# Kernel optimization log

Measured on AMD Instinct MI355X. Metric: run time of the kernel, lower is better.

The kernel has to match this reference:

```python
import jax, jax.numpy as jnp
import numpy as np
import math

RATIO = 0.8

def setup_inputs() -> dict:
    key = jax.random.key(0)
    ks = jax.random.split(key, 10)
    N, E, D = 10000, 320000, 256
    h = jax.random.normal(ks[0], (N, D), dtype=jnp.float32)
    edge_index = jax.random.randint(ks[1], (2, E), 0, N, dtype=jnp.int64)
    s = 1.0 / math.sqrt(D)
    # SAGEConv: lin_l (on aggregated neighbors, with bias), lin_r (on self, no bias)
    W_l = jax.random.normal(ks[2], (D, D), dtype=jnp.float32) * s
    b_l = jax.random.normal(ks[3], (D,), dtype=jnp.float32) * s
    W_r = jax.random.normal(ks[4], (D, D), dtype=jnp.float32) * s
    # SAGPooling score GNN = GraphConv(D, 1): lin_rel (aggr, bias), lin_root (self, no bias)
    W_rel = jax.random.normal(ks[5], (D, 1), dtype=jnp.float32) * s
    b_rel = jax.random.normal(ks[6], (1,), dtype=jnp.float32) * s
    W_root = jax.random.normal(ks[7], (D, 1), dtype=jnp.float32) * s
    # GlobalAttention gate_nn = Linear(D, 1)
    W_gate = jax.random.normal(ks[8], (D, 1), dtype=jnp.float32) * s
    b_gate = jax.random.normal(ks[9], (1,), dtype=jnp.float32) * s
    return {"h": h, "edge_index": edge_index, "W_l": W_l, "b_l": b_l,
            "W_r": W_r, "W_rel": W_rel, "b_rel": b_rel, "W_root": W_root,
            "W_gate": W_gate, "b_gate": b_gate}

def reference(h, edge_index, W_l, b_l, W_r, W_rel, b_rel, W_root, W_gate, b_gate):
    N = h.shape[0]
    src, dst = edge_index[0], edge_index[1]
    # ---- SAGEConv (mean aggregation) ----
    agg = jax.ops.segment_sum(h[src], dst, num_segments=N)          # [N, D]
    deg = jax.ops.segment_sum(jnp.ones_like(dst, dtype=h.dtype), dst, num_segments=N)
    mean = agg / jnp.clip(deg, 1.0)[:, None]
    x = jax.nn.relu(mean @ W_l + b_l + h @ W_r)                     # [N, D]
    # ---- SAGPooling: score via GraphConv (add aggregation), tanh, top-k ----
    s_agg = jax.ops.segment_sum(x[src], dst, num_segments=N)        # [N, D]
    score = (s_agg @ W_rel + b_rel + x @ W_root).reshape(-1)        # [N]
    score = jnp.tanh(score)
    k = int(math.ceil(RATIO * N))                                   # static 8000
    top_score, perm = jax.lax.top_k(score, k)
    xp = x[perm] * top_score[:, None]                               # [k, D]
    # ---- GlobalAttention readout (single graph) ----
    gate = jax.nn.softmax(xp @ W_gate + b_gate, axis=0)             # [k, 1]
    out = jnp.sum(gate * xp, axis=0, keepdims=True)                 # [1, D]
    return out
```

## Files before the change

kernel.cpp:

```cpp
#include <hip/hip_runtime.h>
#include <hip/hip_fp8.h>
#include <math.h>

#define NN 10000
#define NE 320000
#define DD 256
#define KSEL 8000
#define KK 512
#define NPART 157

typedef unsigned int uint;
typedef unsigned short ushort;
typedef unsigned char uchar;
typedef __attribute__((ext_vector_type(8))) short short8;
typedef __attribute__((ext_vector_type(4))) float f32x4;
typedef __attribute__((ext_vector_type(4))) ushort us4;
typedef __attribute__((ext_vector_type(8))) ushort us8;

__device__ __forceinline__ uint encodeF(float f) {
    uint u = __float_as_uint(f);
    return (u & 0x80000000u) ? ~u : (u | 0x80000000u);
}

__device__ __forceinline__ ushort f2bf(float f) {
    uint u = __float_as_uint(f);
    u += 0x7FFFu + ((u >> 16) & 1u);
    return (ushort)(u >> 16);
}

__device__ __forceinline__ float fp8dec(uint b) {
    __hip_fp8_e4m3 t;
    t.__x = (__hip_fp8_storage_t)b;
    return (float)t;
}
__device__ __forceinline__ uint fp8enc(float f) {
    return (uint)__hip_fp8_e4m3(f).__x;
}

#define ZQUADS 2504
__global__ __launch_bounds__(256) void zero_bufs(float4* __restrict__ z) {
    int i = blockIdx.x * 256 + threadIdx.x;
    if (i < ZQUADS) z[i] = make_float4(0.f, 0.f, 0.f, 0.f);
}

#define WB 32
#define HB 2500
#define DB 1250
__global__ __launch_bounds__(256) void prep(
    const float* __restrict__ h, const float* __restrict__ W_l,
    const float* __restrict__ W_r, const int* __restrict__ ei,
    ushort* __restrict__ Ab, uchar* __restrict__ h8,
    ushort* __restrict__ Wt, int* __restrict__ degi) {
    const int b = blockIdx.x, t = threadIdx.x;
    if (b < WB) {
        __shared__ float tile[64][65];
        const int tr = b >> 2, tc = b & 3;
        const int k0 = tr * 64, n0 = tc * 64;
        const int r = t >> 6, c = t & 63;
        const float* Wsrc = (k0 < 256) ? (W_l + (size_t)k0 * DD)
                                       : (W_r + (size_t)(k0 - 256) * DD);
#pragma unroll
        for (int i = 0; i < 16; i++) {
            int row = r + i * 4;
            tile[row][c] = Wsrc[(size_t)row * DD + n0 + c];
        }
        __syncthreads();
#pragma unroll
        for (int i = 0; i < 16; i++) {
            int row = r + i * 4;
            Wt[(size_t)(n0 + row) * KK + k0 + c] = f2bf(tile[c][row]);
        }
    } else if (b < WB + HB) {
        int id = (b - WB) * 256 + t;
        int node = id >> 6, seg = (id & 63) * 4;
        float4 v = *(const float4*)(h + (size_t)node * DD + seg);
        us4 o;
        o[0] = f2bf(v.x); o[1] = f2bf(v.y); o[2] = f2bf(v.z); o[3] = f2bf(v.w);
        *(us4*)(Ab + (size_t)node * KK + 256 + seg) = o;
        uint pk = fp8enc(v.x) | (fp8enc(v.y) << 8)
                | (fp8enc(v.z) << 16) | (fp8enc(v.w) << 24);
        *(uint*)(h8 + (size_t)node * DD + seg) = pk;
    } else {
        int e = (b - WB - HB) * 256 + t;
        if (e < NE) atomicAdd(&degi[ei[NE + e]], 1);
    }
}

__global__ __launch_bounds__(1024) void scan_start(
    const int* __restrict__ degi, int* __restrict__ start,
    int* __restrict__ cursor, float* __restrict__ invdeg) {
    __shared__ int wsum[16];
    __shared__ int woff[16];
    const int t = threadIdx.x, wid = t >> 6, lane = t & 63;
    const int CH = 10;
    const int base = t * CH;
    int sum = 0;
#pragma unroll
    for (int i = 0; i < CH; i++) {
        int idx = base + i;
        if (idx < NN) sum += degi[idx];
    }
    int x = sum;
#pragma unroll
    for (int off = 1; off < 64; off <<= 1) {
        int v = __shfl_up(x, off);
        if (lane >= off) x += v;
    }
    if (lane == 63) wsum[wid] = x;
    __syncthreads();
    if (t == 0) {
        int run = 0;
#pragma unroll
        for (int w = 0; w < 16; w++) { woff[w] = run; run += wsum[w]; }
    }
    __syncthreads();
    int run = woff[wid] + x - sum;
#pragma unroll
    for (int i = 0; i < CH; i++) {
        int idx = base + i;
        if (idx < NN) {
            start[idx]  = run;
            cursor[idx] = run;
            int d = degi[idx];
            invdeg[idx] = 1.0f / fmaxf((float)d, 1.0f);
            run += d;
        }
    }
    if (t == 1023) start[NN] = NE;
}

__global__ __launch_bounds__(256) void fill_csr(
    const int* __restrict__ ei, int* __restrict__ cursor,
    int* __restrict__ csr) {
    int e = blockIdx.x * 256 + threadIdx.x;
    if (e >= NE) return;
    int pos = atomicAdd(&cursor[ei[NE + e]], 1);
    csr[pos] = ei[e];
}

__global__ __launch_bounds__(256) void gather_mean(
    ushort* __restrict__ Ab, const uchar* __restrict__ h8,
    const int* __restrict__ csr,
    const int* __restrict__ start, const float* __restrict__ invdeg) {
    int node = blockIdx.x * 4 + (threadIdx.x >> 6);
    int lane = threadIdx.x & 63;
    if (node >= NN) return;
    int s = start[node], e = start[node + 1];
    const uchar* hp = h8 + lane * 4;
    float a0 = 0.f, a1 = 0.f, a2 = 0.f, a3 = 0.f;
    float b0 = 0.f, b1 = 0.f, b2 = 0.f, b3 = 0.f;
    int j = s;
    for (; j + 4 <= e; j += 4) {
        int s0 = csr[j], s1 = csr[j + 1], s2 = csr[j + 2], s3 = csr[j + 3];
        uint w0 = *(const uint*)(hp + (size_t)s0 * DD);
        uint w1 = *(const uint*)(hp + (size_t)s1 * DD);
        uint w2 = *(const uint*)(hp + (size_t)s2 * DD);
        uint w3 = *(const uint*)(hp + (size_t)s3 * DD);
        a0 += fp8dec(w0 & 0xFF) + fp8dec(w1 & 0xFF);
        a1 += fp8dec((w0 >> 8) & 0xFF) + fp8dec((w1 >> 8) & 0xFF);
        a2 += fp8dec((w0 >> 16) & 0xFF) + fp8dec((w1 >> 16) & 0xFF);
        a3 += fp8dec(w0 >> 24) + fp8dec(w1 >> 24);
        b0 += fp8dec(w2 & 0xFF) + fp8dec(w3 & 0xFF);
        b1 += fp8dec((w2 >> 8) & 0xFF) + fp8dec((w3 >> 8) & 0xFF);
        b2 += fp8dec((w2 >> 16) & 0xFF) + fp8dec((w3 >> 16) & 0xFF);
        b3 += fp8dec(w2 >> 24) + fp8dec(w3 >> 24);
    }
    for (; j < e; j++) {
        uint w0 = *(const uint*)(hp + (size_t)csr[j] * DD);
        a0 += fp8dec(w0 & 0xFF);
        a1 += fp8dec((w0 >> 8) & 0xFF);
        a2 += fp8dec((w0 >> 16) & 0xFF);
        a3 += fp8dec(w0 >> 24);
    }
    float id = invdeg[node];
    us4 m;
    m[0] = f2bf((a0 + b0) * id);
    m[1] = f2bf((a1 + b1) * id);
    m[2] = f2bf((a2 + b2) * id);
    m[3] = f2bf((a3 + b3) * id);
    *(us4*)(Ab + (size_t)node * KK + lane * 4) = m;
}

__global__ __launch_bounds__(256) void gemm_x(
    const ushort* __restrict__ Ab, const ushort* __restrict__ Wt,
    const float* __restrict__ b_l,
    const float* __restrict__ W_rel, const float* __restrict__ W_gate,
    const float* __restrict__ W_root,
    float* __restrict__ xout, float* __restrict__ y,
    float* __restrict__ cvec, float* __restrict__ rvec) {
    __shared__ ushort Asm[2][32][40];
    __shared__ ushort Bsm[2][256][40];
    __shared__ float Ys[4][32], Cs[4][32], Rs[4][32];
    const int t    = threadIdx.x;
    const int row0 = blockIdx.x * 32;
    const int wid  = t >> 6, lane = t & 63;
    const int l15  = lane & 15, g = lane >> 4;

    f32x4 acc[2][4];
#pragma unroll
    for (int fi = 0; fi < 2; fi++)
#pragma unroll
        for (int fj = 0; fj < 4; fj++) acc[fi][fj] = (f32x4)0.f;

    const int  arow = t >> 3, akseg = (t & 7) * 4;
    const bool aok  = (row0 + arow) < NN;
    const ushort* aptr = Ab + (size_t)(row0 + arow) * KK + akseg;
    const ushort* bptr = Wt + (size_t)t * KK;

    us4 areg = {0, 0, 0, 0};
    us8 breg[4];
    if (aok) areg = *(const us4*)(aptr);
#pragma unroll
    for (int jj = 0; jj < 4; jj++) breg[jj] = *(const us8*)(bptr + jj * 8);
    *(us4*)&Asm[0][arow][akseg] = areg;
#pragma unroll
    for (int jj = 0; jj < 4; jj++) *(us8*)&Bsm[0][t][jj * 8] = breg[jj];
    __syncthreads();

    for (int ks = 0; ks < 16; ++ks) {
        const int cur = ks & 1;
        if (ks < 15) {
            const int k0 = (ks + 1) * 32;
            if (aok) areg = *(const us4*)(aptr + k0);
#pragma unroll
            for (int jj = 0; jj < 4; jj++) breg[jj] = *(const us8*)(bptr + k0 + jj * 8);
        }
        short8 af0 = *(const short8*)&Asm[cur][l15][g * 8];
        short8 af1 = *(const short8*)&Asm[cur][16 + l15][g * 8];
#pragma unroll
        for (int fj = 0; fj < 4; fj++) {
            short8 bf = *(const short8*)&Bsm[cur][wid * 64 + fj * 16 + l15][g * 8];
            acc[0][fj] = __builtin_amdgcn_mfma_f32_16x16x32_bf16(af0, bf, acc[0][fj], 0, 0, 0);
            acc[1][fj] = __builtin_amdgcn_mfma_f32_16x16x32_bf16(af1, bf, acc[1][fj], 0, 0, 0);
        }
        if (ks < 15) {
            const int nb = cur ^ 1;
            *(us4*)&Asm[nb][arow][akseg] = areg;
#pragma unroll
            for (int jj = 0; jj < 4; jj++) *(us8*)&Bsm[nb][t][jj * 8] = breg[jj];
        }
        __syncthreads();
    }

    const int wcol0 = wid * 64;
    float bl[4], wl[4], wg[4], wo[4];
#pragma unroll
    for (int fj = 0; fj < 4; fj++) {
        int col = wcol0 + fj * 16 + l15;
        bl[fj] = b_l[col]; wl[fj] = W_rel[col];
        wg[fj] = W_gate[col]; wo[fj] = W_root[col];
    }
#pragma unroll
    for (int fi = 0; fi < 2; fi++) {
#pragma unroll
        for (int r = 0; r < 4; r++) {
            int row = row0 + fi * 16 + g * 4 + r;
            float py = 0.f, pc = 0.f, pr = 0.f;
#pragma unroll
            for (int fj = 0; fj < 4; fj++) {
                float v = fmaxf(acc[fi][fj][r] + bl[fj], 0.f);
                if (row < NN)
                    xout[(size_t)row * DD + wcol0 + fj * 16 + l15] = v;
                py = fmaf(v, wl[fj], py);
                pc = fmaf(v, wg[fj], pc);
                pr = fmaf(v, wo[fj], pr);
            }
#pragma unroll
            for (int off = 1; off < 16; off <<= 1) {
                py += __shfl_xor(py, off);
                pc += __shfl_xor(pc, off);
                pr += __shfl_xor(pr, off);
            }
            if (l15 == 0) {
                int rl = fi * 16 + g * 4 + r;
                Ys[wid][rl] = py; Cs[wid][rl] = pc; Rs[wid][rl] = pr;
            }
        }
    }
    __syncthreads();
    if (t < 32) {
        int row = row0 + t;
        if (row < NN) {
            y[row]    = Ys[0][t] + Ys[1][t] + Ys[2][t] + Ys[3][t];
            cvec[row] = Cs[0][t] + Cs[1][t] + Cs[2][t] + Cs[3][t];
            rvec[row] = Rs[0][t] + Rs[1][t] + Rs[2][t] + Rs[3][t];
        }
    }
}

__global__ __launch_bounds__(256) void gather_score(
    const float* __restrict__ y, const float* __restrict__ r,
    const float* __restrict__ b_rel, const int* __restrict__ csr,
    const int* __restrict__ start,
    float* __restrict__ score, uint* __restrict__ key) {
    int gt   = blockIdx.x * 256 + threadIdx.x;
    int node = gt >> 4, l = gt & 15;
    if (node >= NN) return;
    int s = start[node], e = start[node + 1];
    float acc = 0.f;
    for (int j = s + l; j < e; j += 16) acc += y[csr[j]];
#pragma unroll
    for (int o = 8; o; o >>= 1) acc += __shfl_xor(acc, o, 16);
    if (l == 0) {
        float sc = tanhf(acc + b_rel[0] + r[node]);
        score[node] = sc;
        key[node]   = encodeF(sc);
    }
}

__global__ __launch_bounds__(1024) void radix_select(
    const uint* __restrict__ key, const float* __restrict__ score,
    const float* __restrict__ cvec,
    float* __restrict__ wsc, float* __restrict__ denom) {
    __shared__ uint  hist[16][260];
    __shared__ uint  sh_prefix, sh_need;
    __shared__ float wred[16];
    __shared__ uint  tick_s;
    const int t = threadIdx.x, wid = t >> 6, lane = t & 63;

    uint  myk[10];
    float mys[10], myl[10];
#pragma unroll
    for (int i = 0; i < 10; i++) {
        int idx = t + i * 1024;
        if (idx < NN) {
            uint k  = key[idx];
            float s = score[idx];
            myk[i] = k; mys[i] = s; myl[i] = s * cvec[idx];
        } else {
            myk[i] = 0u; mys[i] = 0.f; myl[i] = -INFINITY;
        }
    }

    uint prefix = 0, pmask = 0, need = KSEL;
    float vmax = -INFINITY;
    for (int shift = 24; shift >= 0; shift -= 8) {
        for (int i = lane; i < 256; i += 64) hist[wid][i] = 0;
        if (shift == 0) {
#pragma unroll
            for (int i = 0; i < 10; i++) {
                uint k = myk[i];
                if ((k & pmask) == prefix) atomicAdd(&hist[wid][k & 255], 1u);
                if (k >= prefix) vmax = fmaxf(vmax, myl[i]);
            }
        } else {
#pragma unroll
            for (int i = 0; i < 10; i++) {
                uint k = myk[i];
                if ((k & pmask) == prefix)
                    atomicAdd(&hist[wid][(k >> shift) & 255], 1u);
            }
        }
        __syncthreads();
        if (wid == 0) {
            uint4 a = make_uint4(0u, 0u, 0u, 0u);
#pragma unroll
            for (int w = 0; w < 16; w++) {
                uint4 v = *(const uint4*)&hist[w][lane * 4];
                a.x += v.x; a.y += v.y; a.z += v.z; a.w += v.w;
            }
            uint s3 = a.w, s2 = a.z + s3, s1 = a.y + s2, s0 = a.x + s1;
            uint x = s0;
#pragma unroll
            for (int off = 1; off < 64; off <<= 1) {
                uint v = __shfl_down(x, off);
                if (lane + off < 64) x += v;
            }
            uint excl = x - s0;
            uint hi0 = excl + s0, hi1 = excl + s1;
            uint hi2 = excl + s2, hi3 = excl + s3;
            if (need <= hi0 && need > hi0 - a.x) {
                sh_prefix = prefix | ((uint)(lane * 4 + 0) << shift);
                sh_need   = need - (hi0 - a.x);
            }
            if (need <= hi1 && need > hi1 - a.y) {
                sh_prefix = prefix | ((uint)(lane * 4 + 1) << shift);
                sh_need   = need - (hi1 - a.y);
            }
            if (need <= hi2 && need > hi2 - a.z) {
                sh_prefix = prefix | ((uint)(lane * 4 + 2) << shift);
                sh_need   = need - (hi2 - a.z);
            }
            if (need <= hi3 && need > hi3 - a.w) {
                sh_prefix = prefix | ((uint)(lane * 4 + 3) << shift);
                sh_need   = need - (hi3 - a.w);
            }
        }
        __syncthreads();
        prefix = sh_prefix;
        need   = sh_need;
        pmask |= (0xFFu << shift);
    }
    const uint T      = prefix;
    const uint needEq = need;
#pragma unroll
    for (int o = 32; o; o >>= 1) vmax = fmaxf(vmax, __shfl_xor(vmax, o));
    if (lane == 0) wred[wid] = vmax;
    if (t == 0) tick_s = 0;
    __syncthreads();
    float m = wred[0];
#pragma unroll
    for (int w = 1; w < 16; w++) m = fmaxf(m, wred[w]);
    __syncthreads();
    float dsum = 0.f;
#pragma unroll
    for (int i = 0; i < 10; i++) {
        int idx = t + i * 1024;
        if (idx >= NN) continue;
        uint k = myk[i];
        bool selm = (k > T);
        if (k == T) selm = (atomicAdd(&tick_s, 1u) < needEq);
        float wv = 0.f;
        if (selm) {
            float w = expf(myl[i] - m);
            wv   = w * mys[i];
            dsum += w;
        }
        wsc[idx] = wv;
    }
#pragma unroll
    for (int o = 32; o; o >>= 1) dsum += __shfl_xor(dsum, o);
    if (lane == 0) wred[wid] = dsum;
    __syncthreads();
    if (t == 0) {
        float d = 0.f;
#pragma unroll
        for (int w = 0; w < 16; w++) d += wred[w];
        denom[0] = d;
    }
}

__global__ __launch_bounds__(256) void reduce_rows(
    const float* __restrict__ x, const float* __restrict__ wsc,
    float* __restrict__ part, uint* __restrict__ counter,
    const float* __restrict__ denom, float* __restrict__ out) {
    __shared__ float red[3][DD];
    __shared__ uint  lastdone;
    const int wave = threadIdx.x >> 6;
    const int lane = threadIdx.x & 63;
    const int row0 = (blockIdx.x * 4 + wave) * 16;
    const float* xp = x + lane * 4;
    float4 acc = make_float4(0.f, 0.f, 0.f, 0.f);
    if (row0 < NN) {
#pragma unroll
        for (int rb = 0; rb < 16; rb += 4) {
            int r0 = row0 + rb;
            float w0 = wsc[r0 + 0], w1 = wsc[r0 + 1];
            float w2 = wsc[r0 + 2], w3 = wsc[r0 + 3];
            float4 v0 = *(const float4*)(xp + (size_t)(r0 + 0) * DD);
            float4 v1 = *(const float4*)(xp + (size_t)(r0 + 1) * DD);
            float4 v2 = *(const float4*)(xp + (size_t)(r0 + 2) * DD);
            float4 v3 = *(const float4*)(xp + (size_t)(r0 + 3) * DD);
            acc.x = fmaf(w0, v0.x, fmaf(w1, v1.x, fmaf(w2, v2.x, fmaf(w3, v3.x, acc.x))));
            acc.y = fmaf(w0, v0.y, fmaf(w1, v1.y, fmaf(w2, v2.y, fmaf(w3, v3.y, acc.y))));
            acc.z = fmaf(w0, v0.z, fmaf(w1, v1.z, fmaf(w2, v2.z, fmaf(w3, v3.z, acc.z))));
            acc.w = fmaf(w0, v0.w, fmaf(w1, v1.w, fmaf(w2, v2.w, fmaf(w3, v3.w, acc.w))));
        }
    }
    if (wave > 0) *(float4*)&red[wave - 1][lane * 4] = acc;
    __syncthreads();
    if (wave == 0) {
#pragma unroll
        for (int w = 0; w < 3; w++) {
            float4 rv = *(float4*)&red[w][lane * 4];
            acc.x += rv.x; acc.y += rv.y; acc.z += rv.z; acc.w += rv.w;
        }
        *(float4*)(part + (size_t)blockIdx.x * DD + lane * 4) = acc;
    }
    __threadfence();
    if (threadIdx.x == 0) lastdone = atomicAdd(counter, 1u);
    __syncthreads();
    if (lastdone == NPART - 1) {
        __threadfence();
        int i = threadIdx.x;
        float s = 0.f;
        for (int b = 0; b < NPART; b++) s += part[(size_t)b * DD + i];
        out[i] = s / denom[0];
    }
}

extern "C" void kernel_launch(void* const* d_in, const int* in_sizes, int n_in,
                              void* d_out, int out_size, void* d_ws, size_t ws_size,
                              hipStream_t stream) {
    const float* h      = (const float*)d_in[0];
    const int*   ei     = (const int*)d_in[1];
    const float* W_l    = (const float*)d_in[2];
    const float* b_l    = (const float*)d_in[3];
    const float* W_r    = (const float*)d_in[4];
    const float* W_rel  = (const float*)d_in[5];
    const float* b_rel  = (const float*)d_in[6];
    const float* W_root = (const float*)d_in[7];
    const float* W_gate = (const float*)d_in[8];
    float* out = (float*)d_out;

    char* p = (char*)d_ws;
    auto alloc = [&p](size_t bytes) {
        char* q = p;
        p += (bytes + 63) & ~(size_t)63;
        return q;
    };
    ushort* Ab    = (ushort*)alloc((size_t)NN * KK * 2);
    uchar*  h8    = (uchar*) alloc((size_t)NN * DD);
    float*  xbuf  = (float*) alloc((size_t)NN * DD * 4);
    ushort* Wt    = (ushort*)alloc((size_t)DD * KK * 2);
    int*    csr   = (int*)   alloc((size_t)NE * 4);
    int*    start = (int*)   alloc((size_t)(NN + 1) * 4);
    int*    cursor= (int*)   alloc((size_t)NN * 4);
    float*  invdeg= (float*) alloc((size_t)NN * 4);
    float*  score = (float*) alloc((size_t)NN * 4);
    uint*   key   = (uint*)  alloc((size_t)NN * 4);
    float*  wsc   = (float*) alloc((size_t)NN * 4);
    float*  denom = (float*) alloc(64);
    float*  part  = (float*) alloc((size_t)NPART * DD * 4);
    float*  y     = (float*) alloc((size_t)NN * 4);
    float*  cbuf  = (float*) alloc((size_t)NN * 4);
    float*  rbuf  = (float*) alloc((size_t)NN * 4);
    int*    degi  = (int*)   alloc((size_t)NN * 4);
    uint*   cnt   = (uint*)  alloc(64);

    zero_bufs   <<<(ZQUADS + 255) / 256, 256, 0, stream>>>((float4*)degi);
    prep        <<<WB + HB + DB, 256, 0, stream>>>(h, W_l, W_r, ei,
                                                   Ab, h8, Wt, degi);
    scan_start  <<<1, 1024, 0, stream>>>(degi, start, cursor, invdeg);
    fill_csr    <<<(NE + 255) / 256, 256, 0, stream>>>(ei, cursor, csr);
    gather_mean <<<(NN + 3) / 4, 256, 0, stream>>>(Ab, h8, csr, start, invdeg);
    gemm_x      <<<(NN + 31) / 32, 256, 0, stream>>>(Ab, Wt, b_l,
                                                     W_rel, W_gate, W_root,
                                                     xbuf, y, cbuf, rbuf);
    gather_score<<<(NN * 16 + 255) / 256, 256, 0, stream>>>(y, rbuf, b_rel, csr,
                                                            start, score, key);
    radix_select<<<1, 1024, 0, stream>>>(key, score, cbuf, wsc, denom);
    reduce_rows <<<NPART, 256, 0, stream>>>(xbuf, wsc, part, cnt, denom, out);
    (void)n_in; (void)in_sizes; (void)out_size; (void)ws_size;
}
```

Before: 161.3 us.

## Fuse neighbor mean gather into the GEMM prologue via shared memory

Removes the separate gather_mean kernel. Each gemm_x block now gathers and averages the fp8 neighbor features for its 32 rows into a shared-memory tile, and the first half of the K loop reads that tile. The self-feature half of the A matrix is still staged from global memory, which is now stored with stride DD instead of KK. This avoids one launch and the global write and re-read of the bf16 mean matrix. In exchange, the latency-bound gather runs with far fewer waves (313 blocks, 8 rows per wave done serially), and the extra shared-memory tile may lower occupancy.

New measurement: 191.3 us. 18.6% more time.

```diff
diff --git a/kernel.cpp b/kernel.cpp
--- a/kernel.cpp
+++ b/kernel.cpp
@@ -76,7 +76,7 @@
         float4 v = *(const float4*)(h + (size_t)node * DD + seg);
         us4 o;
         o[0] = f2bf(v.x); o[1] = f2bf(v.y); o[2] = f2bf(v.z); o[3] = f2bf(v.w);
-        *(us4*)(Ab + (size_t)node * KK + 256 + seg) = o;
+        *(us4*)(Ab + (size_t)node * DD + seg) = o;
         uint pk = fp8enc(v.x) | (fp8enc(v.y) << 8)
                 | (fp8enc(v.z) << 16) | (fp8enc(v.w) << 24);
         *(uint*)(h8 + (size_t)node * DD + seg) = pk;
@@ -138,56 +138,16 @@
     csr[pos] = ei[e];
 }
 
-__global__ __launch_bounds__(256) void gather_mean(
-    ushort* __restrict__ Ab, const uchar* __restrict__ h8,
-    const int* __restrict__ csr,
-    const int* __restrict__ start, const float* __restrict__ invdeg) {
-    int node = blockIdx.x * 4 + (threadIdx.x >> 6);
-    int lane = threadIdx.x & 63;
-    if (node >= NN) return;
-    int s = start[node], e = start[node + 1];
-    const uchar* hp = h8 + lane * 4;
-    float a0 = 0.f, a1 = 0.f, a2 = 0.f, a3 = 0.f;
-    float b0 = 0.f, b1 = 0.f, b2 = 0.f, b3 = 0.f;
-    int j = s;
-    for (; j + 4 <= e; j += 4) {
-        int s0 = csr[j], s1 = csr[j + 1], s2 = csr[j + 2], s3 = csr[j + 3];
-        uint w0 = *(const uint*)(hp + (size_t)s0 * DD);
-        uint w1 = *(const uint*)(hp + (size_t)s1 * DD);
-        uint w2 = *(const uint*)(hp + (size_t)s2 * DD);
-        uint w3 = *(const uint*)(hp + (size_t)s3 * DD);
-        a0 += fp8dec(w0 & 0xFF) + fp8dec(w1 & 0xFF);
-        a1 += fp8dec((w0 >> 8) & 0xFF) + fp8dec((w1 >> 8) & 0xFF);
-        a2 += fp8dec((w0 >> 16) & 0xFF) + fp8dec((w1 >> 16) & 0xFF);
-        a3 += fp8dec(w0 >> 24) + fp8dec(w1 >> 24);
-        b0 += fp8dec(w2 & 0xFF) + fp8dec(w3 & 0xFF);
-        b1 += fp8dec((w2 >> 8) & 0xFF) + fp8dec((w3 >> 8) & 0xFF);
-        b2 += fp8dec((w2 >> 16) & 0xFF) + fp8dec((w3 >> 16) & 0xFF);
-        b3 += fp8dec(w2 >> 24) + fp8dec(w3 >> 24);
-    }
-    for (; j < e; j++) {
-        uint w0 = *(const uint*)(hp + (size_t)csr[j] * DD);
-        a0 += fp8dec(w0 & 0xFF);
-        a1 += fp8dec((w0 >> 8) & 0xFF);
-        a2 += fp8dec((w0 >> 16) & 0xFF);
-        a3 += fp8dec(w0 >> 24);
-    }
-    float id = invdeg[node];
-    us4 m;
-    m[0] = f2bf((a0 + b0) * id);
-    m[1] = f2bf((a1 + b1) * id);
-    m[2] = f2bf((a2 + b2) * id);
-    m[3] = f2bf((a3 + b3) * id);
-    *(us4*)(Ab + (size_t)node * KK + lane * 4) = m;
-}
-
 __global__ __launch_bounds__(256) void gemm_x(
-    const ushort* __restrict__ Ab, const ushort* __restrict__ Wt,
-    const float* __restrict__ b_l,
+    const ushort* __restrict__ Ab, const uchar* __restrict__ h8,
+    const int* __restrict__ csr, const int* __restrict__ start,
+    const float* __restrict__ invdeg,
+    const ushort* __restrict__ Wt, const float* __restrict__ b_l,
     const float* __restrict__ W_rel, const float* __restrict__ W_gate,
     const float* __restrict__ W_root,
     float* __restrict__ xout, float* __restrict__ y,
     float* __restrict__ cvec, float* __restrict__ rvec) {
+    __shared__ ushort Ms[32][264];
     __shared__ ushort Asm[2][32][40];
     __shared__ ushort Bsm[2][256][40];
     __shared__ float Ys[4][32], Cs[4][32], Rs[4][32];
@@ -196,6 +156,50 @@
     const int wid  = t >> 6, lane = t & 63;
     const int l15  = lane & 15, g = lane >> 4;
 
+#pragma unroll
+    for (int rr = 0; rr < 8; ++rr) {
+        const int lrow = wid * 8 + rr;
+        const int row  = row0 + lrow;
+        float a0 = 0.f, a1 = 0.f, a2 = 0.f, a3 = 0.f;
+        float b0 = 0.f, b1 = 0.f, b2 = 0.f, b3 = 0.f;
+        float id = 1.f;
+        if (row < NN) {
+            int s = start[row], e = start[row + 1];
+            id = invdeg[row];
+            const uchar* hp = h8 + lane * 4;
+            int j = s;
+            for (; j + 4 <= e; j += 4) {
+                int s0 = csr[j], s1 = csr[j + 1];
+                int s2 = csr[j + 2], s3 = csr[j + 3];
+                uint w0 = *(const uint*)(hp + (size_t)s0 * DD);
+                uint w1 = *(const uint*)(hp + (size_t)s1 * DD);
+                uint w2 = *(const uint*)(hp + (size_t)s2 * DD);
+                uint w3 = *(const uint*)(hp + (size_t)s3 * DD);
+                a0 += fp8dec(w0 & 0xFF) + fp8dec(w1 & 0xFF);
+                a1 += fp8dec((w0 >> 8) & 0xFF) + fp8dec((w1 >> 8) & 0xFF);
+                a2 += fp8dec((w0 >> 16) & 0xFF) + fp8dec((w1 >> 16) & 0xFF);
+                a3 += fp8dec(w0 >> 24) + fp8dec(w1 >> 24);
+                b0 += fp8dec(w2 & 0xFF) + fp8dec(w3 & 0xFF);
+                b1 += fp8dec((w2 >> 8) & 0xFF) + fp8dec((w3 >> 8) & 0xFF);
+                b2 += fp8dec((w2 >> 16) & 0xFF) + fp8dec((w3 >> 16) & 0xFF);
+                b3 += fp8dec(w2 >> 24) + fp8dec(w3 >> 24);
+            }
+            for (; j < e; j++) {
+                uint w0 = *(const uint*)(hp + (size_t)csr[j] * DD);
+                a0 += fp8dec(w0 & 0xFF);
+                a1 += fp8dec((w0 >> 8) & 0xFF);
+                a2 += fp8dec((w0 >> 16) & 0xFF);
+                a3 += fp8dec(w0 >> 24);
+            }
+        }
+        us4 m;
+        m[0] = f2bf((a0 + b0) * id);
+        m[1] = f2bf((a1 + b1) * id);
+        m[2] = f2bf((a2 + b2) * id);
+        m[3] = f2bf((a3 + b3) * id);
+        *(us4*)&Ms[lrow][lane * 4] = m;
+    }
+
     f32x4 acc[2][4];
 #pragma unroll
     for (int fi = 0; fi < 2; fi++)
@@ -204,29 +208,33 @@
 
     const int  arow = t >> 3, akseg = (t & 7) * 4;
     const bool aok  = (row0 + arow) < NN;
-    const ushort* aptr = Ab + (size_t)(row0 + arow) * KK + akseg;
+    const ushort* aptr = Ab + (size_t)(row0 + arow) * DD + akseg;
     const ushort* bptr = Wt + (size_t)t * KK;
 
     us4 areg = {0, 0, 0, 0};
     us8 breg[4];
-    if (aok) areg = *(const us4*)(aptr);
 #pragma unroll
     for (int jj = 0; jj < 4; jj++) breg[jj] = *(const us8*)(bptr + jj * 8);
-    *(us4*)&Asm[0][arow][akseg] = areg;
 #pragma unroll
     for (int jj = 0; jj < 4; jj++) *(us8*)&Bsm[0][t][jj * 8] = breg[jj];
     __syncthreads();
 
     for (int ks = 0; ks < 16; ++ks) {
         const int cur = ks & 1;
+        const int k0 = (ks + 1) * 32;
         if (ks < 15) {
-            const int k0 = (ks + 1) * 32;
-            if (aok) areg = *(const us4*)(aptr + k0);
 #pragma unroll
             for (int jj = 0; jj < 4; jj++) breg[jj] = *(const us8*)(bptr + k0 + jj * 8);
-        }
-        short8 af0 = *(const short8*)&Asm[cur][l15][g * 8];
-        short8 af1 = *(const short8*)&Asm[cur][16 + l15][g * 8];
+            if (k0 >= 256 && aok) areg = *(const us4*)(aptr + k0 - 256);
+        }
+        short8 af0, af1;
+        if (ks < 8) {
+            af0 = *(const short8*)&Ms[l15][ks * 32 + g * 8];
+            af1 = *(const short8*)&Ms[16 + l15][ks * 32 + g * 8];
+        } else {
+            af0 = *(const short8*)&Asm[cur][l15][g * 8];
+            af1 = *(const short8*)&Asm[cur][16 + l15][g * 8];
+        }
 #pragma unroll
         for (int fj = 0; fj < 4; fj++) {
             short8 bf = *(const short8*)&Bsm[cur][wid * 64 + fj * 16 + l15][g * 8];
@@ -235,9 +243,9 @@
         }
         if (ks < 15) {
             const int nb = cur ^ 1;
-            *(us4*)&Asm[nb][arow][akseg] = areg;
 #pragma unroll
             for (int jj = 0; jj < 4; jj++) *(us8*)&Bsm[nb][t][jj * 8] = breg[jj];
+            if (k0 >= 256) *(us4*)&Asm[nb][arow][akseg] = areg;
         }
         __syncthreads();
     }
@@ -499,7 +507,7 @@
         p += (bytes + 63) & ~(size_t)63;
         return q;
     };
-    ushort* Ab    = (ushort*)alloc((size_t)NN * KK * 2);
+    ushort* Ab    = (ushort*)alloc((size_t)NN * DD * 2);
     uchar*  h8    = (uchar*) alloc((size_t)NN * DD);
     float*  xbuf  = (float*) alloc((size_t)NN * DD * 4);
     ushort* Wt    = (ushort*)alloc((size_t)DD * KK * 2);
@@ -523,8 +531,8 @@
                                                    Ab, h8, Wt, degi);
     scan_start  <<<1, 1024, 0, stream>>>(degi, start, cursor, invdeg);
     fill_csr    <<<(NE + 255) / 256, 256, 0, stream>>>(ei, cursor, csr);
-    gather_mean <<<(NN + 3) / 4, 256, 0, stream>>>(Ab, h8, csr, start, invdeg);
-    gemm_x      <<<(NN + 31) / 32, 256, 0, stream>>>(Ab, Wt, b_l,
+    gemm_x      <<<(NN + 31) / 32, 256, 0, stream>>>(Ab, h8, csr, start, invdeg,
+                                                     Wt, b_l,
                                                      W_rel, W_gate, W_root,
                                                      xbuf, y, cbuf, rbuf);
     gather_score<<<(NN * 16 + 255) / 256, 256, 0, stream>>>(y, rbuf, b_rel, csr,
```
